# Performance work log

Hardware: AMD Instinct MI355X
Metric: run time of the kernel (lower is better)

## Reference

```python
import jax, jax.numpy as jnp
import numpy as np

N0, N1 = 81, 319          # hard-coded split t1[:, :81] / t1[:, 81:]
C_OUT = 64
LAYERS = 5
EPS = 1e-5


def _temporal_conv(X, w1, b1, wc, bc):
    # X: [B, N, T, Cin] -> NCHW with H=N, W=T, kernel (1, 3), VALID
    out_ch = w1.shape[0]
    Xp = jnp.transpose(X, (0, 3, 1, 2))
    dn = ('NCHW', 'OIHW', 'NCHW')
    conv = lambda x, w: jax.lax.conv_general_dilated(x, w, (1, 1), 'VALID', dimension_numbers=dn)
    xc = conv(Xp, wc) + bc[None, :, None, None]
    temp = conv(Xp, w1) + b1[None, :, None, None]
    x_p, x_q = xc[:, :out_ch], xc[:, out_ch:]
    out = (x_p + temp) * jax.nn.sigmoid(x_q)
    return jnp.transpose(out, (0, 2, 3, 1))  # [B, N, T-2, out_ch]


def _het_conv(X0l, X1l, X00, Aaa, Aab, Aba, th1, th2, th3):
    # torch einsum('ij,jklm->kilm', A, X.permute(1,0,2,3)) == einsum('ij,bjtc->bitc', A, X)
    u1 = jnp.einsum('ij,bjtc->bitc', Aaa, X0l)
    u2 = jax.nn.relu(u1 @ th1)
    u3 = jnp.einsum('ij,bjtc->bitc', Aab @ Aba, X0l)
    u4 = jnp.einsum('ij,bjtc->bitc', Aab, X1l)
    u5 = jax.nn.sigmoid(u3 @ th2 + u4 @ th3)
    u6 = jax.nn.relu((u2 + u5) * 0.5)
    return jax.nn.relu(0.9 * u6 + 0.1 * X00)


def setup_inputs() -> dict:
    key = jax.random.key(0)
    ks = jax.random.split(key, 24)
    B, N, T, Cin = 16, 400, 32, 2
    stdv = 1.0 / np.sqrt(C_OUT)
    u = lambda k, shape, s: jax.random.uniform(k, shape, jnp.float32, -s, s)
    inp = {
        'X': jax.random.normal(ks[0], (B, N, T, Cin), jnp.float32),
        'A00': jax.random.uniform(ks[1], (N0, N0), jnp.float32) / N0,
        'A01': jax.random.uniform(ks[2], (N0, N1), jnp.float32) / N1,
        'A10': jax.random.uniform(ks[3], (N1, N0), jnp.float32) / N0,
        'A11': jax.random.uniform(ks[4], (N1, N1), jnp.float32) / N1,
        't1_conv1_w': jax.random.normal(ks[5], (C_OUT, Cin, 1, 3), jnp.float32) * 0.1,
        't1_conv1_b': jnp.zeros((C_OUT,), jnp.float32),
        't1_causal_w': jax.random.normal(ks[6], (2 * C_OUT, Cin, 1, 3), jnp.float32) * 0.1,
        't1_causal_b': jnp.zeros((2 * C_OUT,), jnp.float32),
        'g1_th1': u(ks[7], (LAYERS, C_OUT, C_OUT), stdv),
        'g1_th2': u(ks[8], (LAYERS, C_OUT, C_OUT), stdv),
        'g1_th3': u(ks[9], (LAYERS, C_OUT, C_OUT), stdv),
        'g2_th1': u(ks[10], (LAYERS, C_OUT, C_OUT), stdv),
        'g2_th2': u(ks[11], (LAYERS, C_OUT, C_OUT), stdv),
        'g2_th3': u(ks[12], (LAYERS, C_OUT, C_OUT), stdv),
        'theta': u(ks[13], (C_OUT, C_OUT), stdv),
        't2_conv1_w': jax.random.normal(ks[14], (C_OUT, C_OUT, 1, 3), jnp.float32) * 0.05,
        't2_conv1_b': jnp.zeros((C_OUT,), jnp.float32),
        't2_causal_w': jax.random.normal(ks[15], (2 * C_OUT, C_OUT, 1, 3), jnp.float32) * 0.05,
        't2_causal_b': jnp.zeros((2 * C_OUT,), jnp.float32),
        'bn_gamma': jnp.ones((N,), jnp.float32),
        'bn_beta': jnp.zeros((N,), jnp.float32),
    }
    return inp


def reference(X, A00, A01, A10, A11, t1_conv1_w, t1_conv1_b, t1_causal_w, t1_causal_b,
              g1_th1, g1_th2, g1_th3, g2_th1, g2_th2, g2_th3, theta,
              t2_conv1_w, t2_conv1_b, t2_causal_w, t2_causal_b, bn_gamma, bn_beta):
    t1 = _temporal_conv(X, t1_conv1_w, t1_conv1_b, t1_causal_w, t1_causal_b)  # [B,N,T-2,64]
    X0, X1 = t1[:, :N0], t1[:, N0:]
    u0, u1v = X0, X1
    for i in range(LAYERS):
        u0 = _het_conv(u0, u1v, X0, A00, A01, A10, g1_th1[i], g1_th2[i], g1_th3[i])
        u1v = _het_conv(u1v, u0, X1, A11, A10, A01, g2_th1[i], g2_th2[i], g2_th3[i])
    tk = jnp.concatenate([u0, u1v], axis=1)            # [B,N,T-2,64]
    tk = jax.nn.relu(tk @ theta)
    tk = _temporal_conv(tk, t2_conv1_w, t2_conv1_b, t2_causal_w, t2_causal_b)  # [B,N,T-4,64]
    # BatchNorm2d(num_nodes): channel axis is the node axis (dim 1), training-mode batch stats
    mean = tk.mean(axis=(0, 2, 3), keepdims=True)
    var = tk.var(axis=(0, 2, 3), keepdims=True)
    return (tk - mean) / jnp.sqrt(var + EPS) * bn_gamma[None, :, None, None] + bn_beta[None, :, None, None]
```

## Files before the change

kernel.cpp:

```cpp
#include <hip/hip_runtime.h>


typedef __attribute__((ext_vector_type(8))) short short8v;
typedef __attribute__((ext_vector_type(4))) short short4v;
typedef __attribute__((ext_vector_type(4))) float f32x4;

#define BB 16
#define NA 81
#define NB 319
#define PA 128
#define PB 320
#define M1 1920
#define T1 30
#define T2 28

#define MFMA16 __builtin_amdgcn_mfma_f32_16x16x32_bf16

__device__ __forceinline__ float sigmoidf_(float x){ return 1.0f/(1.0f+__expf(-x)); }
__device__ __forceinline__ short f2bf(float f){
  unsigned u = __float_as_uint(f);
  u += 0x7FFF + ((u>>16)&1);
  return (short)(u>>16);
}
__device__ __forceinline__ float bf2f(short s){
  return __uint_as_float(((unsigned)(unsigned short)s)<<16);
}

__global__ __launch_bounds__(256) void k_prep_mm(const float* __restrict__ A01,
                                                 const float* __restrict__ A10,
                                                 float* __restrict__ Ma) {
  int idx = blockIdx.x*256 + threadIdx.x;
  if (idx >= NA*NA) return;
  int i = idx / NA, j = idx % NA;
  float a = 0.f;
  for (int k = 0; k < NB; ++k) a += A01[i*NB + k]*A10[k*NA + j];
  Ma[idx] = a;
}

__device__ __forceinline__ void packA_one(int f, const float* src, int I, int J,
                                          int ld, int nIt, short* dst) {
  int e = f & 7, l = (f >> 3) & 63, rest = f >> 9;
  int it = rest % nIt, jt = rest / nIt;
  int i = it*16 + (l & 15);
  int j = jt*32 + (l >> 4)*8 + e;
  float v = (i < I && j < J) ? src[i*ld + j] : 0.f;
  dst[f] = f2bf(v);
}

__global__ __launch_bounds__(256) void k_pack_A(
    const float* __restrict__ A00, const float* __restrict__ A01,
    const float* __restrict__ A10, const float* __restrict__ A11,
    const float* __restrict__ Ma,
    short* __restrict__ A00pk, short* __restrict__ Mapk,
    short* __restrict__ A01pk, short* __restrict__ A10pk,
    short* __restrict__ A11pk) {
  int idx = blockIdx.x*256 + threadIdx.x;
  if (idx < 12288)        { packA_one(idx, A00, NA, NA, NA, 8,  A00pk); return; }
  idx -= 12288;
  if (idx < 12288)        { packA_one(idx, Ma,  NA, NA, NA, 8,  Mapk);  return; }
  idx -= 12288;
  if (idx < 40960)        { packA_one(idx, A01, NA, NB, NB, 8,  A01pk); return; }
  idx -= 40960;
  if (idx < 30720)        { packA_one(idx, A10, NB, NA, NA, 20, A10pk); return; }
  idx -= 30720;
  if (idx < 102400)       { packA_one(idx, A11, NB, NB, NB, 20, A11pk); return; }
}

__global__ __launch_bounds__(256) void k_pack_th(
    const float* __restrict__ g1t1, const float* __restrict__ g1t2,
    const float* __restrict__ g1t3, const float* __restrict__ g2t1,
    const float* __restrict__ g2t2, const float* __restrict__ g2t3,
    const float* __restrict__ theta,
    const float* __restrict__ w12, const float* __restrict__ wc2,
    const float* __restrict__ w11, const float* __restrict__ wc1,
    const float* __restrict__ b11, const float* __restrict__ bc1,
    short* __restrict__ thpk, short* __restrict__ thetapk,
    short* __restrict__ W2pk, float* __restrict__ W1t, float* __restrict__ B1t) {
  int idx = blockIdx.x*256 + threadIdx.x;
  if (idx < 122880) {
    int mat = idx / 4096, rem = idx % 4096;
    int ct = rem / 1024, ks = (rem / 512) & 1, l = (rem >> 3) & 63, e = rem & 7;
    int ci = ks*32 + (l >> 4)*8 + e, co = ct*16 + (l & 15);
    int layer = mat / 6, which = mat % 6;
    const float* src = which == 0 ? g1t1 : which == 1 ? g1t2 : which == 2 ? g1t3
                     : which == 3 ? g2t1 : which == 4 ? g2t2 : g2t3;
    thpk[idx] = f2bf(src[layer*4096 + ci*64 + co]);
    return;
  }
  idx -= 122880;
  if (idx < 4096) {
    int ct = idx / 1024, ks = (idx / 512) & 1, l = (idx >> 3) & 63, e = idx & 7;
    int ci = ks*32 + (l >> 4)*8 + e, co = ct*16 + (l & 15);
    thetapk[idx] = f2bf(theta[ci*64 + co]);
    return;
  }
  idx -= 4096;
  if (idx < 36864) {
    int ct = idx / 3072, rem = idx % 3072;
    int ks = rem / 512, l = (rem >> 3) & 63, e = rem & 7;
    int kap = ks*32 + (l >> 4)*8 + e;
    int k = kap >> 6, ci = kap & 63;
    int cc = ct*16 + (l & 15);
    float v = (cc < 64) ? w12[cc*192 + ci*3 + k] : wc2[(cc - 64)*192 + ci*3 + k];
    W2pk[idx] = f2bf(v);
    return;
  }
  idx -= 36864;
  if (idx < 1152) {
    int kk = idx / 192, cc = idx % 192;
    int k = kk >> 1, ci = kk & 1;
    W1t[idx] = (cc < 64) ? w11[cc*6 + ci*3 + k] : wc1[(cc - 64)*6 + ci*3 + k];
    return;
  }
  idx -= 1152;
  if (idx < 192) { B1t[idx] = (idx < 64) ? b11[idx] : bc1[idx - 64]; return; }
}

__global__ __launch_bounds__(192) void k_tconv1(const float* __restrict__ X,
                                                const float* __restrict__ W1t,
                                                const float* __restrict__ B1t,
                                                short* __restrict__ t1a,
                                                short* __restrict__ t1b) {
  __shared__ float xl[64];
  __shared__ float wl[6*192];
  __shared__ float bl[192];
  __shared__ float ol[T1*192];
  int bn = blockIdx.x;
  int b = bn / 400, n = bn % 400;
  int tid = threadIdx.x;
  if (tid < 64) xl[tid] = X[(size_t)bn*64 + tid];
  for (int i2 = tid; i2 < 6*192; i2 += 192) wl[i2] = W1t[i2];
  bl[tid] = B1t[tid];
  __syncthreads();
  float acc[T1];
  float bias = bl[tid];
#pragma unroll
  for (int t = 0; t < T1; ++t) acc[t] = bias;
#pragma unroll
  for (int kk = 0; kk < 6; ++kk) {
    float w = wl[kk*192 + tid];
    int k = kk >> 1, ci = kk & 1;
#pragma unroll
    for (int t = 0; t < T1; ++t) acc[t] += xl[(t + k)*2 + ci]*w;
  }
#pragma unroll
  for (int t = 0; t < T1; ++t) ol[t*192 + tid] = acc[t];
  __syncthreads();
  short* dst = (n < NA) ? (t1a + ((size_t)b*PA + n)*M1)
                        : (t1b + ((size_t)b*PB + (n - NA))*M1);
  for (int p = tid; p < T1*64; p += 192) {
    int t = p >> 6, c = p & 63;
    float v = (ol[t*192 + 64 + c] + ol[t*192 + c])*sigmoidf_(ol[t*192 + 128 + c]);
    dst[p] = f2bf(v);
  }
}

__global__ __launch_bounds__(256) void k_transpose(const short* __restrict__ src,
                                                   short* __restrict__ dst, int Ipad) {
  int lane = threadIdx.x & 63, wv = threadIdx.x >> 6;
  int n = blockIdx.x*64 + lane;
  int b = blockIdx.z;
  const short* sp = src + ((size_t)b*Ipad + n)*M1;
  int mbase = (blockIdx.y*4 + wv)*120;
  for (int k = 0; k < 120; k += 8) {
    int m = mbase + k;
    short8v v = *(const short8v*)(sp + m);
#pragma unroll
    for (int e = 0; e < 8; ++e)
      dst[((size_t)b*M1 + m + e)*Ipad + n] = v[e];
  }
}

template<int KT12, int KT3>
__global__ __launch_bounds__(128, 1) void k_layer_a(
    const short* __restrict__ XT12, int Jp12,
    const short* __restrict__ XT3, int Jp3,
    const short* __restrict__ Apk1, const short* __restrict__ Apk2, int nIt12,
    const short* __restrict__ Apk3, int nIt3,
    const short* __restrict__ th1, const short* __restrict__ th2,
    const short* __restrict__ th3,
    const short* __restrict__ X00, short* __restrict__ uout,
    short* __restrict__ umT, short* __restrict__ g3T,
    int NW, int I, int IpadO) {
  __shared__ short sd[2][3][32*68];
  int lane = threadIdx.x & 63, wv = threadIdx.x >> 6;
  int ln = lane & 15, qw = lane >> 4;

  int total = NW*15*BB;
  int d = blockIdx.x;
  int logical = (d & 7)*(total >> 3) + (d >> 3);
  int w = logical % NW;
  int rest = logical / NW;
  int mt = rest % 15;
  int b = rest / 15;

  int m0 = (mt*2 + wv)*64;
  int t = m0 >> 6;

  short* s1 = sd[wv][0];
  short* s2 = sd[wv][1];
  short* s3 = sd[wv][2];

  short8v x0r[4];
#pragma unroll
  for (int kq = 0; kq < 4; ++kq) {
    int il = kq*8 + (lane >> 3);
    int irow = w*32 + il;
    if (irow >= I) irow = I - 1;
    size_t ro = ((size_t)b*IpadO + irow)*M1 + t*64 + (lane & 7)*8;
    x0r[kq] = *(const short8v*)(X00 + ro);
  }

  {
    f32x4 a3[2][4];
#pragma unroll
    for (int ft = 0; ft < 2; ++ft)
#pragma unroll
      for (int mf = 0; mf < 4; ++mf) a3[ft][mf] = (f32x4)0.f;

    short8v xa[2][4];
    short8v b3f[2][2];
#pragma unroll
    for (int mf = 0; mf < 4; ++mf) {
      size_t ro = ((size_t)b*M1 + m0 + mf*16 + ln)*Jp3 + qw*8;
      xa[0][mf] = *(const short8v*)(XT3 + ro);
    }
    {
      size_t ab = (((size_t)0*nIt3 + w*2)*64 + lane)*8;
      b3f[0][0] = *(const short8v*)(Apk3 + ab);
      b3f[0][1] = *(const short8v*)(Apk3 + ab + 512);
    }
#pragma unroll
    for (int ks = 0; ks < KT3; ++ks) {
      if (ks + 1 < KT3) {
        int nx = (ks + 1) & 1;
#pragma unroll
        for (int mf = 0; mf < 4; ++mf) {
          size_t ro = ((size_t)b*M1 + m0 + mf*16 + ln)*Jp3 + (ks + 1)*32 + qw*8;
          xa[nx][mf] = *(const short8v*)(XT3 + ro);
        }
        size_t ab = (((size_t)(ks + 1)*nIt3 + w*2)*64 + lane)*8;
        b3f[nx][0] = *(const short8v*)(Apk3 + ab);
        b3f[nx][1] = *(const short8v*)(Apk3 + ab + 512);
      }
      int cu = ks & 1;
#pragma unroll
      for (int mf = 0; mf < 4; ++mf) {
        a3[0][mf] = MFMA16(xa[cu][mf], b3f[cu][0], a3[0][mf], 0, 0, 0);
        a3[1][mf] = MFMA16(xa[cu][mf], b3f[cu][1], a3[1][mf], 0, 0, 0);
      }
    }
#pragma unroll
    for (int ft = 0; ft < 2; ++ft)
#pragma unroll
      for (int mf = 0; mf < 4; ++mf) {
        int irow = ft*16 + ln;
        int cc = mf*16 + qw*4;
        short4v v3;
#pragma unroll
        for (int r = 0; r < 4; ++r) v3[r] = f2bf(a3[ft][mf][r]);
        *(short4v*)(s3 + irow*68 + cc) = v3;
      }
  }
  {
    int co = lane;
    size_t cb = ((size_t)b*M1 + t*64 + co)*IpadO + w*32;
#pragma unroll
    for (int kq = 0; kq < 4; ++kq) {
      short8v v;
#pragma unroll
      for (int ii = 0; ii < 8; ++ii) v[ii] = s3[(kq*8 + ii)*68 + co];
      *(short8v*)(g3T + cb + kq*8) = v;
    }
  }

  {
    f32x4 a1[2][4], a2[2][4];
#pragma unroll
    for (int ft = 0; ft < 2; ++ft)
#pragma unroll
      for (int mf = 0; mf < 4; ++mf) { a1[ft][mf] = (f32x4)0.f; a2[ft][mf] = (f32x4)0.f; }

    short8v xa[2][4];
    short8v b1f[2][2], b2f[2][2];
#pragma unroll
    for (int mf = 0; mf < 4; ++mf) {
      size_t ro = ((size_t)b*M1 + m0 + mf*16 + ln)*Jp12 + qw*8;
      xa[0][mf] = *(const short8v*)(XT12 + ro);
    }
    {
      size_t ab = (((size_t)0*nIt12 + w*2)*64 + lane)*8;
      b1f[0][0] = *(const short8v*)(Apk1 + ab);
      b1f[0][1] = *(const short8v*)(Apk1 + ab + 512);
      b2f[0][0] = *(const short8v*)(Apk2 + ab);
      b2f[0][1] = *(const short8v*)(Apk2 + ab + 512);
    }
#pragma unroll
    for (int ks = 0; ks < KT12; ++ks) {
      if (ks + 1 < KT12) {
        int nx = (ks + 1) & 1;
#pragma unroll
        for (int mf = 0; mf < 4; ++mf) {
          size_t ro = ((size_t)b*M1 + m0 + mf*16 + ln)*Jp12 + (ks + 1)*32 + qw*8;
          xa[nx][mf] = *(const short8v*)(XT12 + ro);
        }
        size_t ab = (((size_t)(ks + 1)*nIt12 + w*2)*64 + lane)*8;
        b1f[nx][0] = *(const short8v*)(Apk1 + ab);
        b1f[nx][1] = *(const short8v*)(Apk1 + ab + 512);
        b2f[nx][0] = *(const short8v*)(Apk2 + ab);
        b2f[nx][1] = *(const short8v*)(Apk2 + ab + 512);
      }
      int cu = ks & 1;
#pragma unroll
      for (int mf = 0; mf < 4; ++mf) {
        a1[0][mf] = MFMA16(xa[cu][mf], b1f[cu][0], a1[0][mf], 0, 0, 0);
        a1[1][mf] = MFMA16(xa[cu][mf], b1f[cu][1], a1[1][mf], 0, 0, 0);
        a2[0][mf] = MFMA16(xa[cu][mf], b2f[cu][0], a2[0][mf], 0, 0, 0);
        a2[1][mf] = MFMA16(xa[cu][mf], b2f[cu][1], a2[1][mf], 0, 0, 0);
      }
    }
#pragma unroll
    for (int ft = 0; ft < 2; ++ft)
#pragma unroll
      for (int mf = 0; mf < 4; ++mf) {
        int irow = ft*16 + ln;
        int cc = mf*16 + qw*4;
        short4v v1, v2;
#pragma unroll
        for (int r = 0; r < 4; ++r) {
          v1[r] = f2bf(a1[ft][mf][r]);
          v2[r] = f2bf(a2[ft][mf][r]);
        }
        *(short4v*)(s1 + irow*68 + cc) = v1;
        *(short4v*)(s2 + irow*68 + cc) = v2;
      }
  }

  f32x4 u2a[2][4], u5a[2][4];
#pragma unroll
  for (int fi = 0; fi < 2; ++fi)
#pragma unroll
    for (int ct = 0; ct < 4; ++ct) { u2a[fi][ct] = (f32x4)0.f; u5a[fi][ct] = (f32x4)0.f; }

#pragma unroll
  for (int ks = 0; ks < 2; ++ks) {
    short8v f1[2], f2[2], f3[2];
#pragma unroll
    for (int fi = 0; fi < 2; ++fi) {
      int irow = fi*16 + ln;
      f1[fi] = *(const short8v*)(s1 + irow*68 + ks*32 + qw*8);
      f2[fi] = *(const short8v*)(s2 + irow*68 + ks*32 + qw*8);
      f3[fi] = *(const short8v*)(s3 + irow*68 + ks*32 + qw*8);
    }
#pragma unroll
    for (int ct = 0; ct < 4; ++ct) {
      short8v b1 = *(const short8v*)(th1 + ((ct*2 + ks)*64 + lane)*8);
      short8v b2 = *(const short8v*)(th2 + ((ct*2 + ks)*64 + lane)*8);
      short8v b3 = *(const short8v*)(th3 + ((ct*2 + ks)*64 + lane)*8);
#pragma unroll
      for (int fi = 0; fi < 2; ++fi) {
        u2a[fi][ct] = MFMA16(f1[fi], b1, u2a[fi][ct], 0, 0, 0);
        u5a[fi][ct] = MFMA16(f2[fi], b2, u5a[fi][ct], 0, 0, 0);
        u5a[fi][ct] = MFMA16(f3[fi], b3, u5a[fi][ct], 0, 0, 0);
      }
    }
  }

#pragma unroll
  for (int kq = 0; kq < 4; ++kq) {
    int il = kq*8 + (lane >> 3);
    *(short8v*)(s3 + il*68 + (lane & 7)*8) = x0r[kq];
  }

  short* sg = s1;
#pragma unroll
  for (int fi = 0; fi < 2; ++fi)
#pragma unroll
    for (int ct = 0; ct < 4; ++ct) {
      int co = ct*16 + ln;
#pragma unroll
      for (int r = 0; r < 4; ++r) {
        int il = fi*16 + qw*4 + r;
        int i = w*32 + il;
        short g = 0;
        if (i < I) {
          float u2 = fmaxf(u2a[fi][ct][r], 0.f);
          float u5 = sigmoidf_(u5a[fi][ct][r]);
          float u6 = fmaxf(0.5f*(u2 + u5), 0.f);
          float x0 = bf2f(s3[il*68 + co]);
          g = f2bf(fmaxf(0.9f*u6 + 0.1f*x0, 0.f));
        }
        sg[il*68 + co] = g;
      }
    }

#pragma unroll
  for (int kq = 0; kq < 4; ++kq) {
    int il = kq*8 + (lane >> 3);
    int irow = w*32 + il;
    short8v v = *(const short8v*)(sg + il*68 + (lane & 7)*8);
    if (irow < I)
      *(short8v*)(uout + ((size_t)b*IpadO + irow)*M1 + t*64 + (lane & 7)*8) = v;
  }

  {
    int co = lane;
    size_t cb = ((size_t)b*M1 + t*64 + co)*IpadO + w*32;
#pragma unroll
    for (int kq = 0; kq < 4; ++kq) {
      short8v v;
#pragma unroll
      for (int ii = 0; ii < 8; ++ii) v[ii] = sg[(kq*8 + ii)*68 + co];
      *(short8v*)(umT + cb + kq*8) = v;
    }
  }
}

__global__ __launch_bounds__(128, 1) void k_layer_b(
    const short* __restrict__ X2T,
    const short* __restrict__ X3T,
    const short* __restrict__ X1T,
    const short* __restrict__ ApkS,
    const short* __restrict__ Apk1,
    const short* __restrict__ th1, const short* __restrict__ th2,
    const short* __restrict__ th3,
    const short* __restrict__ X00, short* __restrict__ uout,
    short* __restrict__ umT) {
  const int NW = 10, I = NB, IpadO = PB;
  __shared__ short sd[2][3][32*68];
  int lane = threadIdx.x & 63, wv = threadIdx.x >> 6;
  int ln = lane & 15, qw = lane >> 4;

  int total = NW*15*BB;
  int d = blockIdx.x;
  int logical = (d & 7)*(total >> 3) + (d >> 3);
  int w = logical % NW;
  int rest = logical / NW;
  int mt = rest % 15;
  int b = rest / 15;

  int m0 = (mt*2 + wv)*64;
  int t = m0 >> 6;

  short* s1 = sd[wv][0];
  short* s2 = sd[wv][1];
  short* s3 = sd[wv][2];

  short8v x0r[4];
#pragma unroll
  for (int kq = 0; kq < 4; ++kq) {
    int il = kq*8 + (lane >> 3);
    int irow = w*32 + il;
    if (irow >= I) irow = I - 1;
    size_t ro = ((size_t)b*IpadO + irow)*M1 + t*64 + (lane & 7)*8;
    x0r[kq] = *(const short8v*)(X00 + ro);
  }

  {
    f32x4 a2[2][4], a3[2][4];
#pragma unroll
    for (int ft = 0; ft < 2; ++ft)
#pragma unroll
      for (int mf = 0; mf < 4; ++mf) { a2[ft][mf] = (f32x4)0.f; a3[ft][mf] = (f32x4)0.f; }

    short8v x2[2][4], x3[2][4];
    short8v bf[2][2];
#pragma unroll
    for (int mf = 0; mf < 4; ++mf) {
      size_t ro = ((size_t)b*M1 + m0 + mf*16 + ln)*PA + qw*8;
      x2[0][mf] = *(const short8v*)(X2T + ro);
      x3[0][mf] = *(const short8v*)(X3T + ro);
    }
    {
      size_t ab = (((size_t)0*20 + w*2)*64 + lane)*8;
      bf[0][0] = *(const short8v*)(ApkS + ab);
      bf[0][1] = *(const short8v*)(ApkS + ab + 512);
    }
#pragma unroll
    for (int ks = 0; ks < 3; ++ks) {
      if (ks + 1 < 3) {
        int nx = (ks + 1) & 1;
#pragma unroll
        for (int mf = 0; mf < 4; ++mf) {
          size_t ro = ((size_t)b*M1 + m0 + mf*16 + ln)*PA + (ks + 1)*32 + qw*8;
          x2[nx][mf] = *(const short8v*)(X2T + ro);
          x3[nx][mf] = *(const short8v*)(X3T + ro);
        }
        size_t ab = (((size_t)(ks + 1)*20 + w*2)*64 + lane)*8;
        bf[nx][0] = *(const short8v*)(ApkS + ab);
        bf[nx][1] = *(const short8v*)(ApkS + ab + 512);
      }
      int cu = ks & 1;
#pragma unroll
      for (int mf = 0; mf < 4; ++mf) {
        a2[0][mf] = MFMA16(x2[cu][mf], bf[cu][0], a2[0][mf], 0, 0, 0);
        a2[1][mf] = MFMA16(x2[cu][mf], bf[cu][1], a2[1][mf], 0, 0, 0);
        a3[0][mf] = MFMA16(x3[cu][mf], bf[cu][0], a3[0][mf], 0, 0, 0);
        a3[1][mf] = MFMA16(x3[cu][mf], bf[cu][1], a3[1][mf], 0, 0, 0);
      }
    }
#pragma unroll
    for (int ft = 0; ft < 2; ++ft)
#pragma unroll
      for (int mf = 0; mf < 4; ++mf) {
        int irow = ft*16 + ln;
        int cc = mf*16 + qw*4;
        short4v v2, v3;
#pragma unroll
        for (int r = 0; r < 4; ++r) {
          v2[r] = f2bf(a2[ft][mf][r]);
          v3[r] = f2bf(a3[ft][mf][r]);
        }
        *(short4v*)(s2 + irow*68 + cc) = v2;
        *(short4v*)(s3 + irow*68 + cc) = v3;
      }
  }

  {
    f32x4 a1[2][4];
#pragma unroll
    for (int ft = 0; ft < 2; ++ft)
#pragma unroll
      for (int mf = 0; mf < 4; ++mf) a1[ft][mf] = (f32x4)0.f;

    short8v xa[2][4];
    short8v b1f[2][2];
#pragma unroll
    for (int mf = 0; mf < 4; ++mf) {
      size_t ro = ((size_t)b*M1 + m0 + mf*16 + ln)*PB + qw*8;
      xa[0][mf] = *(const short8v*)(X1T + ro);
    }
    {
      size_t ab = (((size_t)0*20 + w*2)*64 + lane)*8;
      b1f[0][0] = *(const short8v*)(Apk1 + ab);
      b1f[0][1] = *(const short8v*)(Apk1 + ab + 512);
    }
#pragma unroll
    for (int ks = 0; ks < 10; ++ks) {
      if (ks + 1 < 10) {
        int nx = (ks + 1) & 1;
#pragma unroll
        for (int mf = 0; mf < 4; ++mf) {
          size_t ro = ((size_t)b*M1 + m0 + mf*16 + ln)*PB + (ks + 1)*32 + qw*8;
          xa[nx][mf] = *(const short8v*)(X1T + ro);
        }
        size_t ab = (((size_t)(ks + 1)*20 + w*2)*64 + lane)*8;
        b1f[nx][0] = *(const short8v*)(Apk1 + ab);
        b1f[nx][1] = *(const short8v*)(Apk1 + ab + 512);
      }
      int cu = ks & 1;
#pragma unroll
      for (int mf = 0; mf < 4; ++mf) {
        a1[0][mf] = MFMA16(xa[cu][mf], b1f[cu][0], a1[0][mf], 0, 0, 0);
        a1[1][mf] = MFMA16(xa[cu][mf], b1f[cu][1], a1[1][mf], 0, 0, 0);
      }
    }
#pragma unroll
    for (int ft = 0; ft < 2; ++ft)
#pragma unroll
      for (int mf = 0; mf < 4; ++mf) {
        int irow = ft*16 + ln;
        int cc = mf*16 + qw*4;
        short4v v1;
#pragma unroll
        for (int r = 0; r < 4; ++r) v1[r] = f2bf(a1[ft][mf][r]);
        *(short4v*)(s1 + irow*68 + cc) = v1;
      }
  }

  f32x4 u2a[2][4], u5a[2][4];
#pragma unroll
  for (int fi = 0; fi < 2; ++fi)
#pragma unroll
    for (int ct = 0; ct < 4; ++ct) { u2a[fi][ct] = (f32x4)0.f; u5a[fi][ct] = (f32x4)0.f; }

#pragma unroll
  for (int ks = 0; ks < 2; ++ks) {
    short8v f1[2], f2[2], f3[2];
#pragma unroll
    for (int fi = 0; fi < 2; ++fi) {
      int irow = fi*16 + ln;
      f1[fi] = *(const short8v*)(s1 + irow*68 + ks*32 + qw*8);
      f2[fi] = *(const short8v*)(s2 + irow*68 + ks*32 + qw*8);
      f3[fi] = *(const short8v*)(s3 + irow*68 + ks*32 + qw*8);
    }
#pragma unroll
    for (int ct = 0; ct < 4; ++ct) {
      short8v b1 = *(const short8v*)(th1 + ((ct*2 + ks)*64 + lane)*8);
      short8v b2 = *(const short8v*)(th2 + ((ct*2 + ks)*64 + lane)*8);
      short8v b3 = *(const short8v*)(th3 + ((ct*2 + ks)*64 + lane)*8);
#pragma unroll
      for (int fi = 0; fi < 2; ++fi) {
        u2a[fi][ct] = MFMA16(f1[fi], b1, u2a[fi][ct], 0, 0, 0);
        u5a[fi][ct] = MFMA16(f2[fi], b2, u5a[fi][ct], 0, 0, 0);
        u5a[fi][ct] = MFMA16(f3[fi], b3, u5a[fi][ct], 0, 0, 0);
      }
    }
  }

#pragma unroll
  for (int kq = 0; kq < 4; ++kq) {
    int il = kq*8 + (lane >> 3);
    *(short8v*)(s3 + il*68 + (lane & 7)*8) = x0r[kq];
  }

  short* sg = s1;
#pragma unroll
  for (int fi = 0; fi < 2; ++fi)
#pragma unroll
    for (int ct = 0; ct < 4; ++ct) {
      int co = ct*16 + ln;
#pragma unroll
      for (int r = 0; r < 4; ++r) {
        int il = fi*16 + qw*4 + r;
        int i = w*32 + il;
        short g = 0;
        if (i < I) {
          float u2 = fmaxf(u2a[fi][ct][r], 0.f);
          float u5 = sigmoidf_(u5a[fi][ct][r]);
          float u6 = fmaxf(0.5f*(u2 + u5), 0.f);
          float x0 = bf2f(s3[il*68 + co]);
          g = f2bf(fmaxf(0.9f*u6 + 0.1f*x0, 0.f));
        }
        sg[il*68 + co] = g;
      }
    }

#pragma unroll
  for (int kq = 0; kq < 4; ++kq) {
    int il = kq*8 + (lane >> 3);
    int irow = w*32 + il;
    short8v v = *(const short8v*)(sg + il*68 + (lane & 7)*8);
    if (irow < I)
      *(short8v*)(uout + ((size_t)b*IpadO + irow)*M1 + t*64 + (lane & 7)*8) = v;
  }

  {
    int co = lane;
    size_t cb = ((size_t)b*M1 + t*64 + co)*IpadO + w*32;
#pragma unroll
    for (int kq = 0; kq < 4; ++kq) {
      short8v v;
#pragma unroll
      for (int ii = 0; ii < 8; ++ii) v[ii] = sg[(kq*8 + ii)*68 + co];
      *(short8v*)(umT + cb + kq*8) = v;
    }
  }
}

__global__ __launch_bounds__(256) void k_thconv2(const short* __restrict__ u0,
                                                 const short* __restrict__ u1,
                                                 const short* __restrict__ thetapk,
                                                 const short* __restrict__ W2pk,
                                                 const float* __restrict__ b12,
                                                 const float* __restrict__ bc2,
                                                 float* __restrict__ out) {
  __shared__ short lds[34*72];
  int tid = threadIdx.x, lane = tid & 63, wv = tid >> 6;
  int ln = lane & 15, qw = lane >> 4;
  int bn = blockIdx.x;
  int b = blockIdx.y;
  const short* u; int i, Ipad;
  if (bn < NA) { u = u0; i = bn; Ipad = PA; }
  else         { u = u1; i = bn - NA; Ipad = PB; }
  for (int z = tid; z < 4*72; z += 256) lds[30*72 + z] = 0;

  f32x4 ac[2];
  ac[0] = (f32x4)0.f; ac[1] = (f32x4)0.f;
  size_t ubase = ((size_t)b*Ipad + i)*M1;
#pragma unroll
  for (int ks = 0; ks < 2; ++ks) {
    short8v bm = *(const short8v*)(thetapk + ((wv*2 + ks)*64 + lane)*8);
#pragma unroll
    for (int tf = 0; tf < 2; ++tf) {
      short8v af = *(const short8v*)(u + ubase + (tf*16 + ln)*64 + ks*32 + qw*8);
      ac[tf] = MFMA16(af, bm, ac[tf], 0, 0, 0);
    }
  }
#pragma unroll
  for (int tf = 0; tf < 2; ++tf)
#pragma unroll
    for (int r = 0; r < 4; ++r) {
      int t = tf*16 + qw*4 + r;
      if (t < T1) lds[t*72 + wv*16 + ln] = f2bf(fmaxf(ac[tf][r], 0.f));
    }
  __syncthreads();

  f32x4 a3[2][3];
#pragma unroll
  for (int tf = 0; tf < 2; ++tf)
#pragma unroll
    for (int s = 0; s < 3; ++s) a3[tf][s] = (f32x4)0.f;
  for (int ks = 0; ks < 6; ++ks) {
    short8v af[2];
#pragma unroll
    for (int tf = 0; tf < 2; ++tf) {
      int m = (tf*16 + ln)*64 + ks*32 + qw*8;
      af[tf] = *(const short8v*)(lds + (m >> 6)*72 + (m & 63));
    }
#pragma unroll
    for (int s = 0; s < 3; ++s) {
      int ct = wv + s*4;
      short8v bm = *(const short8v*)(W2pk + ((ct*6 + ks)*64 + lane)*8);
#pragma unroll
      for (int tf = 0; tf < 2; ++tf)
        a3[tf][s] = MFMA16(af[tf], bm, a3[tf][s], 0, 0, 0);
    }
  }
  int co = wv*16 + ln;
  float btm = b12[co], bp = bc2[co], bq = bc2[64 + co];
#pragma unroll
  for (int tf = 0; tf < 2; ++tf)
#pragma unroll
    for (int r = 0; r < 4; ++r) {
      int t = tf*16 + qw*4 + r;
      if (t >= T2) continue;
      float tm = a3[tf][0][r] + btm;
      float p  = a3[tf][1][r] + bp;
      float q  = a3[tf][2][r] + bq;
      out[((size_t)(b*400 + bn)*T2 + t)*64 + co] = (p + tm)*sigmoidf_(q);
    }
}

__global__ __launch_bounds__(256) void k_bn_stats(const float* __restrict__ y,
                                                  float* __restrict__ stats) {
  int n = blockIdx.x;
  int tid = threadIdx.x;
  float s = 0.f, ss = 0.f;
  for (int b = 0; b < BB; ++b) {
    const float* p = y + ((size_t)(b*400 + n))*(T2*64);
    for (int i2 = tid; i2 < T2*64; i2 += 256) {
      float v = p[i2];
      s += v; ss += v*v;
    }
  }
  __shared__ float rs[4], rss[4];
  for (int off = 32; off > 0; off >>= 1) {
    s += __shfl_down(s, off);
    ss += __shfl_down(ss, off);
  }
  if ((tid & 63) == 0) { rs[tid >> 6] = s; rss[tid >> 6] = ss; }
  __syncthreads();
  if (tid == 0) {
    float S = rs[0] + rs[1] + rs[2] + rs[3];
    float SS = rss[0] + rss[1] + rss[2] + rss[3];
    float mean = S/28672.f;
    float var = SS/28672.f - mean*mean;
    stats[n] = mean;
    stats[400 + n] = rsqrtf(var + 1e-5f);
  }
}

__global__ void k_bn_apply(float* __restrict__ y, const float* __restrict__ stats,
                           const float* __restrict__ gamma, const float* __restrict__ beta) {
  int idx = blockIdx.x*blockDim.x + threadIdx.x;
  const int total = BB*400*T2*64/4;
  for (; idx < total; idx += gridDim.x*blockDim.x) {
    int e = idx*4;
    int n = (e/(T2*64)) % 400;
    float mean = stats[n];
    float g = gamma[n]*stats[400 + n];
    float bt = beta[n];
    float4 v = ((float4*)y)[idx];
    v.x = (v.x - mean)*g + bt;
    v.y = (v.y - mean)*g + bt;
    v.z = (v.z - mean)*g + bt;
    v.w = (v.w - mean)*g + bt;
    ((float4*)y)[idx] = v;
  }
}

extern "C" void kernel_launch(void* const* d_in, const int* in_sizes, int n_in,
                              void* d_out, int out_size, void* d_ws, size_t ws_size,
                              hipStream_t stream) {
  const float* X     = (const float*)d_in[0];
  const float* A00   = (const float*)d_in[1];
  const float* A01   = (const float*)d_in[2];
  const float* A10   = (const float*)d_in[3];
  const float* A11   = (const float*)d_in[4];
  const float* w11   = (const float*)d_in[5];
  const float* b11   = (const float*)d_in[6];
  const float* wc1   = (const float*)d_in[7];
  const float* bc1   = (const float*)d_in[8];
  const float* g1t1  = (const float*)d_in[9];
  const float* g1t2  = (const float*)d_in[10];
  const float* g1t3  = (const float*)d_in[11];
  const float* g2t1  = (const float*)d_in[12];
  const float* g2t2  = (const float*)d_in[13];
  const float* g2t3  = (const float*)d_in[14];
  const float* theta = (const float*)d_in[15];
  const float* w12   = (const float*)d_in[16];
  const float* b12   = (const float*)d_in[17];
  const float* wc2   = (const float*)d_in[18];
  const float* bc2   = (const float*)d_in[19];
  const float* gamma = (const float*)d_in[20];
  const float* beta  = (const float*)d_in[21];

  short* ws = (short*)d_ws;
  size_t o = 0;
  const size_t szA = (size_t)BB*PA*M1;
  const size_t szB = (size_t)BB*PB*M1;
  short* t1a  = ws + o; o += szA;
  short* t1b  = ws + o; o += szB;
  short* u0   = ws + o; o += szA;
  short* u1   = ws + o; o += szB;
  short* uaT0 = ws + o; o += szA;
  short* uaT1 = ws + o; o += szA;
  short* ubT0 = ws + o; o += szB;
  short* ubT1 = ws + o; o += szB;
  short* g3T  = ws + o; o += szA;
  short* A00pk = ws + o; o += 12288;
  short* Mapk  = ws + o; o += 12288;
  short* A01pk = ws + o; o += 40960;
  short* A10pk = ws + o; o += 30720;
  short* A11pk = ws + o; o += 102400;
  short* thpk    = ws + o; o += 122880;
  short* thetapk = ws + o; o += 4096;
  short* W2pk    = ws + o; o += 36864;
  o = (o + 7) & ~(size_t)7;
  float* fws = (float*)(ws + o);
  float* Ma    = fws;
  float* stats = Ma + 6561;
  float* W1t   = stats + 800;
  float* B1t   = W1t + 1152;

  k_prep_mm<<<26, 256, 0, stream>>>(A01, A10, Ma);
  k_pack_A<<<776, 256, 0, stream>>>(A00, A01, A10, A11, Ma,
                                    A00pk, Mapk, A01pk, A10pk, A11pk);
  k_pack_th<<<646, 256, 0, stream>>>(g1t1, g1t2, g1t3, g2t1, g2t2, g2t3, theta,
                                     w12, wc2, w11, wc1, b11, bc1,
                                     thpk, thetapk, W2pk, W1t, B1t);
  k_tconv1<<<BB*400, 192, 0, stream>>>(X, W1t, B1t, t1a, t1b);
  k_transpose<<<dim3(PA/64, 4, BB), 256, 0, stream>>>(t1a, uaT0, PA);
  k_transpose<<<dim3(PB/64, 4, BB), 256, 0, stream>>>(t1b, ubT0, PB);

  short* uaT[2] = {uaT0, uaT1};
  short* ubT[2] = {ubT0, ubT1};
  for (int l = 0; l < 5; ++l) {
    int pin = l & 1, pout = 1 - pin;
    const short* th = thpk + (size_t)(l*6)*4096;
    k_layer_a<3, 10><<<720, 128, 0, stream>>>(
        uaT[pin], PA, ubT[pin], PB, A00pk, Mapk, 8, A01pk, 8,
        th + 0*4096, th + 1*4096, th + 2*4096, t1a, u0, uaT[pout], g3T,
        3, NA, PA);
    k_layer_b<<<2400, 128, 0, stream>>>(
        g3T, uaT[pout], ubT[pin], A10pk, A11pk,
        th + 3*4096, th + 4*4096, th + 5*4096, t1b, u1, ubT[pout]);
  }

  k_thconv2<<<dim3(400, BB), 256, 0, stream>>>(u0, u1, thetapk, W2pk, b12, bc2,
                                               (float*)d_out);
  k_bn_stats<<<400, 256, 0, stream>>>((float*)d_out, stats);
  k_bn_apply<<<2048, 256, 0, stream>>>((float*)d_out, stats, gamma, beta);
}
```

Measured before the change: 537.0 us.

## Halve per-wave output-row tile in layer kernels and double grid with higher occupancy

The layer kernels now give each wave 16 output nodes instead of 32, so the accumulator arrays shrink and the shared-memory staging is halved. The grid is doubled to cover the same work, and launch bounds now ask for 4 blocks per CU instead of 1. The aim is more resident waves to hide global-load latency in these memory-bound GEMM-like loops. In exchange, every streamed X tile is read by twice as many waves, which doubles activation traffic and lowers MFMA reuse per load.

```diff
diff --git a/kernel.cpp b/kernel.cpp
--- a/kernel.cpp
+++ b/kernel.cpp
@@ -172,7 +172,7 @@
 }
 
 template<int KT12, int KT3>
-__global__ __launch_bounds__(128, 1) void k_layer_a(
+__global__ __launch_bounds__(128, 4) void k_layer_a(
     const short* __restrict__ XT12, int Jp12,
     const short* __restrict__ XT3, int Jp3,
     const short* __restrict__ Apk1, const short* __restrict__ Apk2, int nIt12,
@@ -182,7 +182,7 @@
     const short* __restrict__ X00, short* __restrict__ uout,
     short* __restrict__ umT, short* __restrict__ g3T,
     int NW, int I, int IpadO) {
-  __shared__ short sd[2][3][32*68];
+  __shared__ short sd[2][3][16*68];
   int lane = threadIdx.x & 63, wv = threadIdx.x >> 6;
   int ln = lane & 15, qw = lane >> 4;
 
@@ -201,35 +201,28 @@
   short* s2 = sd[wv][1];
   short* s3 = sd[wv][2];
 
-  short8v x0r[4];
-#pragma unroll
-  for (int kq = 0; kq < 4; ++kq) {
+  short8v x0r[2];
+#pragma unroll
+  for (int kq = 0; kq < 2; ++kq) {
     int il = kq*8 + (lane >> 3);
-    int irow = w*32 + il;
+    int irow = w*16 + il;
     if (irow >= I) irow = I - 1;
     size_t ro = ((size_t)b*IpadO + irow)*M1 + t*64 + (lane & 7)*8;
     x0r[kq] = *(const short8v*)(X00 + ro);
   }
 
   {
-    f32x4 a3[2][4];
-#pragma unroll
-    for (int ft = 0; ft < 2; ++ft)
-#pragma unroll
-      for (int mf = 0; mf < 4; ++mf) a3[ft][mf] = (f32x4)0.f;
-
+    f32x4 a3[4];
+#pragma unroll
+    for (int mf = 0; mf < 4; ++mf) a3[mf] = (f32x4)0.f;
     short8v xa[2][4];
-    short8v b3f[2][2];
+    short8v b3f[2];
 #pragma unroll
     for (int mf = 0; mf < 4; ++mf) {
       size_t ro = ((size_t)b*M1 + m0 + mf*16 + ln)*Jp3 + qw*8;
       xa[0][mf] = *(const short8v*)(XT3 + ro);
     }
-    {
-      size_t ab = (((size_t)0*nIt3 + w*2)*64 + lane)*8;
-      b3f[0][0] = *(const short8v*)(Apk3 + ab);
-      b3f[0][1] = *(const short8v*)(Apk3 + ab + 512);
-    }
+    b3f[0] = *(const short8v*)(Apk3 + (((size_t)0*nIt3 + w)*64 + lane)*8);
 #pragma unroll
     for (int ks = 0; ks < KT3; ++ks) {
       if (ks + 1 < KT3) {
@@ -239,34 +232,27 @@
           size_t ro = ((size_t)b*M1 + m0 + mf*16 + ln)*Jp3 + (ks + 1)*32 + qw*8;
           xa[nx][mf] = *(const short8v*)(XT3 + ro);
         }
-        size_t ab = (((size_t)(ks + 1)*nIt3 + w*2)*64 + lane)*8;
-        b3f[nx][0] = *(const short8v*)(Apk3 + ab);
-        b3f[nx][1] = *(const short8v*)(Apk3 + ab + 512);
+        b3f[nx] = *(const short8v*)(Apk3 + (((size_t)(ks + 1)*nIt3 + w)*64 + lane)*8);
       }
       int cu = ks & 1;
 #pragma unroll
-      for (int mf = 0; mf < 4; ++mf) {
-        a3[0][mf] = MFMA16(xa[cu][mf], b3f[cu][0], a3[0][mf], 0, 0, 0);
-        a3[1][mf] = MFMA16(xa[cu][mf], b3f[cu][1], a3[1][mf], 0, 0, 0);
-      }
-    }
-#pragma unroll
-    for (int ft = 0; ft < 2; ++ft)
-#pragma unroll
-      for (int mf = 0; mf < 4; ++mf) {
-        int irow = ft*16 + ln;
-        int cc = mf*16 + qw*4;
-        short4v v3;
-#pragma unroll
-        for (int r = 0; r < 4; ++r) v3[r] = f2bf(a3[ft][mf][r]);
-        *(short4v*)(s3 + irow*68 + cc) = v3;
-      }
+      for (int mf = 0; mf < 4; ++mf)
+        a3[mf] = MFMA16(xa[cu][mf], b3f[cu], a3[mf], 0, 0, 0);
+    }
+#pragma unroll
+    for (int mf = 0; mf < 4; ++mf) {
+      int cc = mf*16 + qw*4;
+      short4v v3;
+#pragma unroll
+      for (int r = 0; r < 4; ++r) v3[r] = f2bf(a3[mf][r]);
+      *(short4v*)(s3 + ln*68 + cc) = v3;
+    }
   }
   {
     int co = lane;
-    size_t cb = ((size_t)b*M1 + t*64 + co)*IpadO + w*32;
-#pragma unroll
-    for (int kq = 0; kq < 4; ++kq) {
+    size_t cb = ((size_t)b*M1 + t*64 + co)*IpadO + w*16;
+#pragma unroll
+    for (int kq = 0; kq < 2; ++kq) {
       short8v v;
 #pragma unroll
       for (int ii = 0; ii < 8; ++ii) v[ii] = s3[(kq*8 + ii)*68 + co];
@@ -275,26 +261,18 @@
   }
 
   {
-    f32x4 a1[2][4], a2[2][4];
-#pragma unroll
-    for (int ft = 0; ft < 2; ++ft)
-#pragma unroll
-      for (int mf = 0; mf < 4; ++mf) { a1[ft][mf] = (f32x4)0.f; a2[ft][mf] = (f32x4)0.f; }
-
+    f32x4 a1[4], a2[4];
+#pragma unroll
+    for (int mf = 0; mf < 4; ++mf) { a1[mf] = (f32x4)0.f; a2[mf] = (f32x4)0.f; }
     short8v xa[2][4];
-    short8v b1f[2][2], b2f[2][2];
+    short8v b1f[2], b2f[2];
 #pragma unroll
     for (int mf = 0; mf < 4; ++mf) {
       size_t ro = ((size_t)b*M1 + m0 + mf*16 + ln)*Jp12 + qw*8;
       xa[0][mf] = *(const short8v*)(XT12 + ro);
     }
-    {
-      size_t ab = (((size_t)0*nIt12 + w*2)*64 + lane)*8;
-      b1f[0][0] = *(const short8v*)(Apk1 + ab);
-      b1f[0][1] = *(const short8v*)(Apk1 + ab + 512);
-      b2f[0][0] = *(const short8v*)(Apk2 + ab);
-      b2f[0][1] = *(const short8v*)(Apk2 + ab + 512);
-    }
+    b1f[0] = *(const short8v*)(Apk1 + (((size_t)0*nIt12 + w)*64 + lane)*8);
+    b2f[0] = *(const short8v*)(Apk2 + (((size_t)0*nIt12 + w)*64 + lane)*8);
 #pragma unroll
     for (int ks = 0; ks < KT12; ++ks) {
       if (ks + 1 < KT12) {
@@ -304,100 +282,79 @@
           size_t ro = ((size_t)b*M1 + m0 + mf*16 + ln)*Jp12 + (ks + 1)*32 + qw*8;
           xa[nx][mf] = *(const short8v*)(XT12 + ro);
         }
-        size_t ab = (((size_t)(ks + 1)*nIt12 + w*2)*64 + lane)*8;
-        b1f[nx][0] = *(const short8v*)(Apk1 + ab);
-        b1f[nx][1] = *(const short8v*)(Apk1 + ab + 512);
-        b2f[nx][0] = *(const short8v*)(Apk2 + ab);
-        b2f[nx][1] = *(const short8v*)(Apk2 + ab + 512);
+        b1f[nx] = *(const short8v*)(Apk1 + (((size_t)(ks + 1)*nIt12 + w)*64 + lane)*8);
+        b2f[nx] = *(const short8v*)(Apk2 + (((size_t)(ks + 1)*nIt12 + w)*64 + lane)*8);
       }
       int cu = ks & 1;
 #pragma unroll
       for (int mf = 0; mf < 4; ++mf) {
-        a1[0][mf] = MFMA16(xa[cu][mf], b1f[cu][0], a1[0][mf], 0, 0, 0);
-        a1[1][mf] = MFMA16(xa[cu][mf], b1f[cu][1], a1[1][mf], 0, 0, 0);
-        a2[0][mf] = MFMA16(xa[cu][mf], b2f[cu][0], a2[0][mf], 0, 0, 0);
-        a2[1][mf] = MFMA16(xa[cu][mf], b2f[cu][1], a2[1][mf], 0, 0, 0);
-      }
-    }
-#pragma unroll
-    for (int ft = 0; ft < 2; ++ft)
-#pragma unroll
-      for (int mf = 0; mf < 4; ++mf) {
-        int irow = ft*16 + ln;
-        int cc = mf*16 + qw*4;
-        short4v v1, v2;
-#pragma unroll
-        for (int r = 0; r < 4; ++r) {
-          v1[r] = f2bf(a1[ft][mf][r]);
-          v2[r] = f2bf(a2[ft][mf][r]);
-        }
-        *(short4v*)(s1 + irow*68 + cc) = v1;
-        *(short4v*)(s2 + irow*68 + cc) = v2;
-      }
-  }
-
-  f32x4 u2a[2][4], u5a[2][4];
-#pragma unroll
-  for (int fi = 0; fi < 2; ++fi)
-#pragma unroll
-    for (int ct = 0; ct < 4; ++ct) { u2a[fi][ct] = (f32x4)0.f; u5a[fi][ct] = (f32x4)0.f; }
-
+        a1[mf] = MFMA16(xa[cu][mf], b1f[cu], a1[mf], 0, 0, 0);
+        a2[mf] = MFMA16(xa[cu][mf], b2f[cu], a2[mf], 0, 0, 0);
+      }
+    }
+#pragma unroll
+    for (int mf = 0; mf < 4; ++mf) {
+      int cc = mf*16 + qw*4;
+      short4v v1, v2;
+#pragma unroll
+      for (int r = 0; r < 4; ++r) {
+        v1[r] = f2bf(a1[mf][r]);
+        v2[r] = f2bf(a2[mf][r]);
+      }
+      *(short4v*)(s1 + ln*68 + cc) = v1;
+      *(short4v*)(s2 + ln*68 + cc) = v2;
+    }
+  }
+
+  f32x4 u2a[4], u5a[4];
+#pragma unroll
+  for (int ct = 0; ct < 4; ++ct) { u2a[ct] = (f32x4)0.f; u5a[ct] = (f32x4)0.f; }
 #pragma unroll
   for (int ks = 0; ks < 2; ++ks) {
-    short8v f1[2], f2[2], f3[2];
-#pragma unroll
-    for (int fi = 0; fi < 2; ++fi) {
-      int irow = fi*16 + ln;
-      f1[fi] = *(const short8v*)(s1 + irow*68 + ks*32 + qw*8);
-      f2[fi] = *(const short8v*)(s2 + irow*68 + ks*32 + qw*8);
-      f3[fi] = *(const short8v*)(s3 + irow*68 + ks*32 + qw*8);
-    }
+    short8v f1 = *(const short8v*)(s1 + ln*68 + ks*32 + qw*8);
+    short8v f2 = *(const short8v*)(s2 + ln*68 + ks*32 + qw*8);
+    short8v f3 = *(const short8v*)(s3 + ln*68 + ks*32 + qw*8);
 #pragma unroll
     for (int ct = 0; ct < 4; ++ct) {
       short8v b1 = *(const short8v*)(th1 + ((ct*2 + ks)*64 + lane)*8);
       short8v b2 = *(const short8v*)(th2 + ((ct*2 + ks)*64 + lane)*8);
       short8v b3 = *(const short8v*)(th3 + ((ct*2 + ks)*64 + lane)*8);
-#pragma unroll
-      for (int fi = 0; fi < 2; ++fi) {
-        u2a[fi][ct] = MFMA16(f1[fi], b1, u2a[fi][ct], 0, 0, 0);
-        u5a[fi][ct] = MFMA16(f2[fi], b2, u5a[fi][ct], 0, 0, 0);
-        u5a[fi][ct] = MFMA16(f3[fi], b3, u5a[fi][ct], 0, 0, 0);
-      }
-    }
-  }
-
-#pragma unroll
-  for (int kq = 0; kq < 4; ++kq) {
+      u2a[ct] = MFMA16(f1, b1, u2a[ct], 0, 0, 0);
+      u5a[ct] = MFMA16(f2, b2, u5a[ct], 0, 0, 0);
+      u5a[ct] = MFMA16(f3, b3, u5a[ct], 0, 0, 0);
+    }
+  }
+
+#pragma unroll
+  for (int kq = 0; kq < 2; ++kq) {
     int il = kq*8 + (lane >> 3);
     *(short8v*)(s3 + il*68 + (lane & 7)*8) = x0r[kq];
   }
 
   short* sg = s1;
 #pragma unroll
-  for (int fi = 0; fi < 2; ++fi)
-#pragma unroll
-    for (int ct = 0; ct < 4; ++ct) {
-      int co = ct*16 + ln;
-#pragma unroll
-      for (int r = 0; r < 4; ++r) {
-        int il = fi*16 + qw*4 + r;
-        int i = w*32 + il;
-        short g = 0;
-        if (i < I) {
-          float u2 = fmaxf(u2a[fi][ct][r], 0.f);
-          float u5 = sigmoidf_(u5a[fi][ct][r]);
-          float u6 = fmaxf(0.5f*(u2 + u5), 0.f);
-          float x0 = bf2f(s3[il*68 + co]);
-          g = f2bf(fmaxf(0.9f*u6 + 0.1f*x0, 0.f));
-        }
-        sg[il*68 + co] = g;
-      }
-    }
-
-#pragma unroll
-  for (int kq = 0; kq < 4; ++kq) {
+  for (int ct = 0; ct < 4; ++ct) {
+    int co = ct*16 + ln;
+#pragma unroll
+    for (int r = 0; r < 4; ++r) {
+      int il = qw*4 + r;
+      int i = w*16 + il;
+      short g = 0;
+      if (i < I) {
+        float u2 = fmaxf(u2a[ct][r], 0.f);
+        float u5 = sigmoidf_(u5a[ct][r]);
+        float u6 = fmaxf(0.5f*(u2 + u5), 0.f);
+        float x0 = bf2f(s3[il*68 + co]);
+        g = f2bf(fmaxf(0.9f*u6 + 0.1f*x0, 0.f));
+      }
+      sg[il*68 + co] = g;
+    }
+  }
+
+#pragma unroll
+  for (int kq = 0; kq < 2; ++kq) {
     int il = kq*8 + (lane >> 3);
-    int irow = w*32 + il;
+    int irow = w*16 + il;
     short8v v = *(const short8v*)(sg + il*68 + (lane & 7)*8);
     if (irow < I)
       *(short8v*)(uout + ((size_t)b*IpadO + irow)*M1 + t*64 + (lane & 7)*8) = v;
@@ -405,9 +362,9 @@
 
   {
     int co = lane;
-    size_t cb = ((size_t)b*M1 + t*64 + co)*IpadO + w*32;
-#pragma unroll
-    for (int kq = 0; kq < 4; ++kq) {
+    size_t cb = ((size_t)b*M1 + t*64 + co)*IpadO + w*16;
+#pragma unroll
+    for (int kq = 0; kq < 2; ++kq) {
       short8v v;
 #pragma unroll
       for (int ii = 0; ii < 8; ++ii) v[ii] = sg[(kq*8 + ii)*68 + co];
@@ -416,7 +373,7 @@
   }
 }
 
-__global__ __launch_bounds__(128, 1) void k_layer_b(
+__global__ __launch_bounds__(128, 4) void k_layer_b(
     const short* __restrict__ X2T,
     const short* __restrict__ X3T,
     const short* __restrict__ X1T,
@@ -426,8 +383,8 @@
     const short* __restrict__ th3,
     const short* __restrict__ X00, short* __restrict__ uout,
     short* __restrict__ umT) {
-  const int NW = 10, I = NB, IpadO = PB;
-  __shared__ short sd[2][3][32*68];
+  const int NW = 20, I = NB, IpadO = PB;
+  __shared__ short sd[2][3][16*68];
   int lane = threadIdx.x & 63, wv = threadIdx.x >> 6;
   int ln = lane & 15, qw = lane >> 4;
 
@@ -446,36 +403,29 @@
   short* s2 = sd[wv][1];
   short* s3 = sd[wv][2];
 
-  short8v x0r[4];
-#pragma unroll
-  for (int kq = 0; kq < 4; ++kq) {
+  short8v x0r[2];
+#pragma unroll
+  for (int kq = 0; kq < 2; ++kq) {
     int il = kq*8 + (lane >> 3);
-    int irow = w*32 + il;
+    int irow = w*16 + il;
     if (irow >= I) irow = I - 1;
     size_t ro = ((size_t)b*IpadO + irow)*M1 + t*64 + (lane & 7)*8;
     x0r[kq] = *(const short8v*)(X00 + ro);
   }
 
   {
-    f32x4 a2[2][4], a3[2][4];
-#pragma unroll
-    for (int ft = 0; ft < 2; ++ft)
-#pragma unroll
-      for (int mf = 0; mf < 4; ++mf) { a2[ft][mf] = (f32x4)0.f; a3[ft][mf] = (f32x4)0.f; }
-
+    f32x4 a2[4], a3[4];
+#pragma unroll
+    for (int mf = 0; mf < 4; ++mf) { a2[mf] = (f32x4)0.f; a3[mf] = (f32x4)0.f; }
     short8v x2[2][4], x3[2][4];
-    short8v bf[2][2];
+    short8v bf[2];
 #pragma unroll
     for (int mf = 0; mf < 4; ++mf) {
       size_t ro = ((size_t)b*M1 + m0 + mf*16 + ln)*PA + qw*8;
       x2[0][mf] = *(const short8v*)(X2T + ro);
       x3[0][mf] = *(const short8v*)(X3T + ro);
     }
-    {
-      size_t ab = (((size_t)0*20 + w*2)*64 + lane)*8;
-      bf[0][0] = *(const short8v*)(ApkS + ab);
-      bf[0][1] = *(const short8v*)(ApkS + ab + 512);
-    }
+    bf[0] = *(const short8v*)(ApkS + (((size_t)0*20 + w)*64 + lane)*8);
 #pragma unroll
     for (int ks = 0; ks < 3; ++ks) {
       if (ks + 1 < 3) {
@@ -486,55 +436,41 @@
           x2[nx][mf] = *(const short8v*)(X2T + ro);
           x3[nx][mf] = *(const short8v*)(X3T + ro);
         }
-        size_t ab = (((size_t)(ks + 1)*20 + w*2)*64 + lane)*8;
-        bf[nx][0] = *(const short8v*)(ApkS + ab);
-        bf[nx][1] = *(const short8v*)(ApkS + ab + 512);
+        bf[nx] = *(const short8v*)(ApkS + (((size_t)(ks + 1)*20 + w)*64 + lane)*8);
       }
       int cu = ks & 1;
 #pragma unroll
       for (int mf = 0; mf < 4; ++mf) {
-        a2[0][mf] = MFMA16(x2[cu][mf], bf[cu][0], a2[0][mf], 0, 0, 0);
-        a2[1][mf] = MFMA16(x2[cu][mf], bf[cu][1], a2[1][mf], 0, 0, 0);
-        a3[0][mf] = MFMA16(x3[cu][mf], bf[cu][0], a3[0][mf], 0, 0, 0);
-        a3[1][mf] = MFMA16(x3[cu][mf], bf[cu][1], a3[1][mf], 0, 0, 0);
-      }
-    }
-#pragma unroll
-    for (int ft = 0; ft < 2; ++ft)
-#pragma unroll
-      for (int mf = 0; mf < 4; ++mf) {
-        int irow = ft*16 + ln;
-        int cc = mf*16 + qw*4;
-        short4v v2, v3;
-#pragma unroll
-        for (int r = 0; r < 4; ++r) {
-          v2[r] = f2bf(a2[ft][mf][r]);
-          v3[r] = f2bf(a3[ft][mf][r]);
-        }
-        *(short4v*)(s2 + irow*68 + cc) = v2;
-        *(short4v*)(s3 + irow*68 + cc) = v3;
-      }
+        a2[mf] = MFMA16(x2[cu][mf], bf[cu], a2[mf], 0, 0, 0);
+        a3[mf] = MFMA16(x3[cu][mf], bf[cu], a3[mf], 0, 0, 0);
+      }
+    }
+#pragma unroll
+    for (int mf = 0; mf < 4; ++mf) {
+      int cc = mf*16 + qw*4;
+      short4v v2, v3;
+#pragma unroll
+      for (int r = 0; r < 4; ++r) {
+        v2[r] = f2bf(a2[mf][r]);
+        v3[r] = f2bf(a3[mf][r]);
+      }
+      *(short4v*)(s2 + ln*68 + cc) = v2;
+      *(short4v*)(s3 + ln*68 + cc) = v3;
+    }
   }
 
   {
-    f32x4 a1[2][4];
-#pragma unroll
-    for (int ft = 0; ft < 2; ++ft)
-#pragma unroll
-      for (int mf = 0; mf < 4; ++mf) a1[ft][mf] = (f32x4)0.f;
-
+    f32x4 a1[4];
+#pragma unroll
+    for (int mf = 0; mf < 4; ++mf) a1[mf] = (f32x4)0.f;
     short8v xa[2][4];
-    short8v b1f[2][2];
+    short8v b1f[2];
 #pragma unroll
     for (int mf = 0; mf < 4; ++mf) {
       size_t ro = ((size_t)b*M1 + m0 + mf*16 + ln)*PB + qw*8;
       xa[0][mf] = *(const short8v*)(X1T + ro);
     }
-    {
-      size_t ab = (((size_t)0*20 + w*2)*64 + lane)*8;
-      b1f[0][0] = *(const short8v*)(Apk1 + ab);
-      b1f[0][1] = *(const short8v*)(Apk1 + ab + 512);
-    }
+    b1f[0] = *(const short8v*)(Apk1 + (((size_t)0*20 + w)*64 + lane)*8);
 #pragma unroll
     for (int ks = 0; ks < 10; ++ks) {
       if (ks + 1 < 10) {
@@ -544,92 +480,72 @@
           size_t ro = ((size_t)b*M1 + m0 + mf*16 + ln)*PB + (ks + 1)*32 + qw*8;
           xa[nx][mf] = *(const short8v*)(X1T + ro);
         }
-        size_t ab = (((size_t)(ks + 1)*20 + w*2)*64 + lane)*8;
-        b1f[nx][0] = *(const short8v*)(Apk1 + ab);
-        b1f[nx][1] = *(const short8v*)(Apk1 + ab + 512);
+        b1f[nx] = *(const short8v*)(Apk1 + (((size_t)(ks + 1)*20 + w)*64 + lane)*8);
       }
       int cu = ks & 1;
 #pragma unroll
-      for (int mf = 0; mf < 4; ++mf) {
-        a1[0][mf] = MFMA16(xa[cu][mf], b1f[cu][0], a1[0][mf], 0, 0, 0);
-        a1[1][mf] = MFMA16(xa[cu][mf], b1f[cu][1], a1[1][mf], 0, 0, 0);
-      }
-    }
-#pragma unroll
-    for (int ft = 0; ft < 2; ++ft)
-#pragma unroll
-      for (int mf = 0; mf < 4; ++mf) {
-        int irow = ft*16 + ln;
-        int cc = mf*16 + qw*4;
-        short4v v1;
-#pragma unroll
-        for (int r = 0; r < 4; ++r) v1[r] = f2bf(a1[ft][mf][r]);
-        *(short4v*)(s1 + irow*68 + cc) = v1;
-      }
-  }
-
-  f32x4 u2a[2][4], u5a[2][4];
-#pragma unroll
-  for (int fi = 0; fi < 2; ++fi)
-#pragma unroll
-    for (int ct = 0; ct < 4; ++ct) { u2a[fi][ct] = (f32x4)0.f; u5a[fi][ct] = (f32x4)0.f; }
-
+      for (int mf = 0; mf < 4; ++mf)
+        a1[mf] = MFMA16(xa[cu][mf], b1f[cu], a1[mf], 0, 0, 0);
+    }
+#pragma unroll
+    for (int mf = 0; mf < 4; ++mf) {
+      int cc = mf*16 + qw*4;
+      short4v v1;
+#pragma unroll
+      for (int r = 0; r < 4; ++r) v1[r] = f2bf(a1[mf][r]);
+      *(short4v*)(s1 + ln*68 + cc) = v1;
+    }
+  }
+
+  f32x4 u2a[4], u5a[4];
+#pragma unroll
+  for (int ct = 0; ct < 4; ++ct) { u2a[ct] = (f32x4)0.f; u5a[ct] = (f32x4)0.f; }
 #pragma unroll
   for (int ks = 0; ks < 2; ++ks) {
-    short8v f1[2], f2[2], f3[2];
-#pragma unroll
-    for (int fi = 0; fi < 2; ++fi) {
-      int irow = fi*16 + ln;
-      f1[fi] = *(const short8v*)(s1 + irow*68 + ks*32 + qw*8);
-      f2[fi] = *(const short8v*)(s2 + irow*68 + ks*32 + qw*8);
-      f3[fi] = *(const short8v*)(s3 + irow*68 + ks*32 + qw*8);
-    }
+    short8v f1 = *(const short8v*)(s1 + ln*68 + ks*32 + qw*8);
+    short8v f2 = *(const short8v*)(s2 + ln*68 + ks*32 + qw*8);
+    short8v f3 = *(const short8v*)(s3 + ln*68 + ks*32 + qw*8);
 #pragma unroll
     for (int ct = 0; ct < 4; ++ct) {
       short8v b1 = *(const short8v*)(th1 + ((ct*2 + ks)*64 + lane)*8);
       short8v b2 = *(const short8v*)(th2 + ((ct*2 + ks)*64 + lane)*8);
       short8v b3 = *(const short8v*)(th3 + ((ct*2 + ks)*64 + lane)*8);
-#pragma unroll
-      for (int fi = 0; fi < 2; ++fi) {
-        u2a[fi][ct] = MFMA16(f1[fi], b1, u2a[fi][ct], 0, 0, 0);
-        u5a[fi][ct] = MFMA16(f2[fi], b2, u5a[fi][ct], 0, 0, 0);
-        u5a[fi][ct] = MFMA16(f3[fi], b3, u5a[fi][ct], 0, 0, 0);
-      }
-    }
-  }
-
-#pragma unroll
-  for (int kq = 0; kq < 4; ++kq) {
+      u2a[ct] = MFMA16(f1, b1, u2a[ct], 0, 0, 0);
+      u5a[ct] = MFMA16(f2, b2, u5a[ct], 0, 0, 0);
+      u5a[ct] = MFMA16(f3, b3, u5a[ct], 0, 0, 0);
+    }
+  }
+
+#pragma unroll
+  for (int kq = 0; kq < 2; ++kq) {
     int il = kq*8 + (lane >> 3);
     *(short8v*)(s3 + il*68 + (lane & 7)*8) = x0r[kq];
   }
 
   short* sg = s1;
 #pragma unroll
-  for (int fi = 0; fi < 2; ++fi)
-#pragma unroll
-    for (int ct = 0; ct < 4; ++ct) {
-      int co = ct*16 + ln;
-#pragma unroll
-      for (int r = 0; r < 4; ++r) {
-        int il = fi*16 + qw*4 + r;
-        int i = w*32 + il;
-        short g = 0;
-        if (i < I) {
-          float u2 = fmaxf(u2a[fi][ct][r], 0.f);
-          float u5 = sigmoidf_(u5a[fi][ct][r]);
-          float u6 = fmaxf(0.5f*(u2 + u5), 0.f);
-          float x0 = bf2f(s3[il*68 + co]);
-          g = f2bf(fmaxf(0.9f*u6 + 0.1f*x0, 0.f));
-        }
-        sg[il*68 + co] = g;
-      }
-    }
-
-#pragma unroll
-  for (int kq = 0; kq < 4; ++kq) {
+  for (int ct = 0; ct < 4; ++ct) {
+    int co = ct*16 + ln;
+#pragma unroll
+    for (int r = 0; r < 4; ++r) {
+      int il = qw*4 + r;
+      int i = w*16 + il;
+      short g = 0;
+      if (i < I) {
+        float u2 = fmaxf(u2a[ct][r], 0.f);
+        float u5 = sigmoidf_(u5a[ct][r]);
+        float u6 = fmaxf(0.5f*(u2 + u5), 0.f);
+        float x0 = bf2f(s3[il*68 + co]);
+        g = f2bf(fmaxf(0.9f*u6 + 0.1f*x0, 0.f));
+      }
+      sg[il*68 + co] = g;
+    }
+  }
+
+#pragma unroll
+  for (int kq = 0; kq < 2; ++kq) {
     int il = kq*8 + (lane >> 3);
-    int irow = w*32 + il;
+    int irow = w*16 + il;
     short8v v = *(const short8v*)(sg + il*68 + (lane & 7)*8);
     if (irow < I)
       *(short8v*)(uout + ((size_t)b*IpadO + irow)*M1 + t*64 + (lane & 7)*8) = v;
@@ -637,9 +553,9 @@
 
   {
     int co = lane;
-    size_t cb = ((size_t)b*M1 + t*64 + co)*IpadO + w*32;
-#pragma unroll
-    for (int kq = 0; kq < 4; ++kq) {
+    size_t cb = ((size_t)b*M1 + t*64 + co)*IpadO + w*16;
+#pragma unroll
+    for (int kq = 0; kq < 2; ++kq) {
       short8v v;
 #pragma unroll
       for (int ii = 0; ii < 8; ++ii) v[ii] = sg[(kq*8 + ii)*68 + co];
@@ -839,11 +755,11 @@
   for (int l = 0; l < 5; ++l) {
     int pin = l & 1, pout = 1 - pin;
     const short* th = thpk + (size_t)(l*6)*4096;
-    k_layer_a<3, 10><<<720, 128, 0, stream>>>(
+    k_layer_a<3, 10><<<1440, 128, 0, stream>>>(
         uaT[pin], PA, ubT[pin], PB, A00pk, Mapk, 8, A01pk, 8,
         th + 0*4096, th + 1*4096, th + 2*4096, t1a, u0, uaT[pout], g3T,
-        3, NA, PA);
-    k_layer_b<<<2400, 128, 0, stream>>>(
+        6, NA, PA);
+    k_layer_b<<<4800, 128, 0, stream>>>(
         g3T, uaT[pout], ubT[pin], A10pk, A11pk,
         th + 3*4096, th + 4*4096, th + 5*4096, t1b, u1, ubT[pout]);
   }
```

New measurement: 726.9 us. 35.4% more time.
